# Kernel optimization log

Hardware: AMD Instinct MI355X
Metric: run time of the kernel (lower is better)

## Reference

```python
import jax, jax.numpy as jnp
from jax import lax
import numpy as np

T = 131072  # trajectory length


def _model_matrices():
    # F: constant-velocity model on augmented state [pose_t; pose_{t-1}]
    I6 = jnp.eye(6, dtype=jnp.float32)
    F = jnp.zeros((12, 12), dtype=jnp.float32)
    F = F.at[:6, :6].set(2.0 * I6)
    F = F.at[:6, 6:].set(-I6)
    F = F.at[6:, :6].set(I6)
    G = jnp.zeros((12, 6), dtype=jnp.float32)
    G = G.at[:6, :6].set(I6)
    return F, G


def setup_inputs() -> dict:
    key = jax.random.key(0)
    k1, = jax.random.split(key, 1)
    pose_measurements = jax.random.normal(k1, (T, 6), dtype=jnp.float32)
    # SPD noise covariances (scaled identities, as typical in the repo's config)
    process_noise_cov = 0.01 * jnp.eye(6, dtype=jnp.float32)
    measure_noise_cov = 0.05 * jnp.eye(6, dtype=jnp.float32)
    cov_init = jnp.eye(12, dtype=jnp.float32)  # _covariance_matrix_pred buffer
    return {
        "pose_measurements": pose_measurements,
        "process_noise_cov": process_noise_cov,
        "measure_noise_cov": measure_noise_cov,
        "cov_init": cov_init,
    }


def reference(pose_measurements, process_noise_cov, measure_noise_cov, cov_init):
    F, G = _model_matrices()
    Q_aug = G @ process_noise_cov @ G.T  # [[Q, 0], [0, 0]]  (12,12)
    I12 = jnp.eye(12, dtype=jnp.float32)
    z6 = jnp.zeros((12, 6), dtype=jnp.float32)

    def step(carry, meas):
        est, P = carry  # est: (12,), P: (12,12)
        # _predict
        v = est[:6] - est[6:]
        pred = jnp.concatenate([est[:6] + v, est[:6]])  # (12,)
        Pp = F @ P @ F.T + Q_aug
        # _update
        S = Pp[:6, :6] + measure_noise_cov            # (6,6)
        K = Pp[:, :6] @ jnp.linalg.inv(S)             # (12,6)
        est_new = pred + K @ (meas - pred[:6])        # (12,)
        KH = jnp.concatenate([K, z6], axis=1)         # (12,12)
        P_new = (I12 - KH) @ Pp
        return (est_new, P_new), (pred, est_new)

    # rows 0,1 initialized from measurements
    row0 = jnp.concatenate([pose_measurements[0], jnp.zeros(6, dtype=jnp.float32)])
    row1 = jnp.concatenate([pose_measurements[1], pose_measurements[0]])

    (_, _), (preds, ests) = lax.scan(step, (row1, cov_init), pose_measurements[2:])

    head = jnp.stack([row0, row1])                   # (2,12)
    pose_estimate = jnp.concatenate([head, ests], axis=0)    # (T,12)
    pose_prediction = jnp.concatenate([head, preds], axis=0)  # (T,12)
    velocity_estimate = pose_estimate[1:-1, :6] - pose_estimate[1:-1, 6:]

    return (pose_estimate[:, :6], pose_prediction[:, :6], velocity_estimate)
```

## Files before the change

kernel.cpp:

```cpp
#include <hip/hip_runtime.h>

#define T_LEN   131072
#define NSTEPS  (T_LEN - 2)
#define CHUNK   16
#define NCHUNK  8192
#define NCJ     (NCHUNK * 6)
#define CAP     512
#define CPB     128
#define NBLK    (NCHUNK / CPB)
#define K2T     (CPB * 6)

#define OFF_STEADY 16
#define OFF_K1     32
#define OFF_K2     (OFF_K1 + CAP * 4)
#define OFF_LP     (OFF_K2 + CAP * 4)
#define OFF_BT     (OFF_LP + NCHUNK * 16 * 4)
#define OFF_BI     (OFF_BT + NBLK * 16 * 4)

__global__ __launch_bounds__(64) void k_gains(
    const float* __restrict__ pnc, const float* __restrict__ mnc,
    const float* __restrict__ cov, float* __restrict__ ws_f,
    int* __restrict__ ws_i) {
    if (threadIdx.x != 0 || blockIdx.x != 0) return;
    float q = pnc[0];
    float r = mnc[0];
    float a = cov[0];
    float b = cov[6];
    float c = cov[6 * 12 + 6];
    float* k1a = ws_f + OFF_K1 / 4;
    float* k2a = ws_f + OFF_K2 / 4;
    float pk1 = -1e30f, pk2 = -1e30f;
    float k1 = 0.f, k2 = 0.f;
    int stable = 0;
    int s;
    for (s = 0; s < CAP; ++s) {
        float bp = 2.0f * a - b;
        float t2 = 2.0f * b - c;
        float ap = 2.0f * bp - t2 + q;
        float cp = a;
        float S  = ap + r;
        float invS = 1.0f / S;
        k1 = ap * invS;
        k2 = bp * invS;
        k1a[s] = k1;
        k2a[s] = k2;
        float om = 1.0f - k1;
        a = om * ap;
        b = om * bp;
        c = cp - k2 * bp;
        if (fabsf(k1 - pk1) <= 5e-7f * fabsf(k1) &&
            fabsf(k2 - pk2) <= 5e-7f * (fabsf(k2) + 1e-20f)) {
            if (++stable >= 8) { ++s; break; }
        } else {
            stable = 0;
        }
        pk1 = k1; pk2 = k2;
    }
    ws_i[0] = s;
    ws_f[OFF_STEADY / 4]     = k1;
    ws_f[OFF_STEADY / 4 + 1] = k2;
}

__device__ __forceinline__ void load_gains(int s, int sc, const float* k1a,
                                           const float* k2a, float k1s, float k2s,
                                           float& g1, float& g2) {
    int si = (s < sc) ? s : 0;
    float a = k1a[si], b = k2a[si];
    g1 = (s < sc) ? a : k1s;
    g2 = (s < sc) ? b : k2s;
}

__global__ __launch_bounds__(K2T) void k_chunk_scan(
    const float* __restrict__ meas, const float* __restrict__ ws_f,
    const int* __restrict__ ws_i, float* __restrict__ lp,
    float* __restrict__ btot) {
    __shared__ float lm[CPB][5];
    __shared__ float lu[CPB][13];
    int tid = threadIdx.x;
    int cl = tid / 6;
    int j  = tid - 6 * cl;
    int b  = blockIdx.x;
    int c  = b * CPB + cl;
    int sc = ws_i[0];
    float k1s = ws_f[OFF_STEADY / 4], k2s = ws_f[OFF_STEADY / 4 + 1];
    const float* k1a = ws_f + OFF_K1 / 4;
    const float* k2a = ws_f + OFF_K2 / 4;
    int s0 = c * CHUNK;
    float m00 = 1.f, m01 = 0.f, m10 = 0.f, m11 = 1.f;
    float u0 = 0.f, u1 = 0.f;
#pragma unroll
    for (int i = 0; i < CHUNK; ++i) {
        int s = s0 + i;
        if (s < NSTEPS) {
            float g1, g2;
            load_gains(s, sc, k1a, k2a, k1s, k2s, g1, g2);
            float om  = 1.0f - g1;
            float a00 = 2.0f * om, a01 = -om;
            float a10 = 1.0f - 2.0f * g2, a11 = g2;
            float n00 = a00 * m00 + a01 * m10;
            float n01 = a00 * m01 + a01 * m11;
            float n10 = a10 * m00 + a11 * m10;
            float n11 = a10 * m01 + a11 * m11;
            m00 = n00; m01 = n01; m10 = n10; m11 = n11;
            float mj = meas[(s + 2) * 6 + j];
            float v0 = a00 * u0 + a01 * u1 + g1 * mj;
            float v1 = a10 * u0 + a11 * u1 + g2 * mj;
            u0 = v0; u1 = v1;
        }
    }
    if (j == 0) { lm[cl][0] = m00; lm[cl][1] = m01; lm[cl][2] = m10; lm[cl][3] = m11; }
    lu[cl][j] = u0; lu[cl][6 + j] = u1;
    __syncthreads();
    for (int off = 1; off < CPB; off <<= 1) {
        bool act = (cl >= off);
        float M0, M1, M2, M3, P0, P1, P2, P3, pu0, pu1;
        if (act) {
            M0 = lm[cl][0]; M1 = lm[cl][1]; M2 = lm[cl][2]; M3 = lm[cl][3];
            P0 = lm[cl - off][0]; P1 = lm[cl - off][1];
            P2 = lm[cl - off][2]; P3 = lm[cl - off][3];
            pu0 = lu[cl - off][j]; pu1 = lu[cl - off][6 + j];
        }
        __syncthreads();
        if (act) {
            float nu0 = M0 * pu0 + M1 * pu1 + u0;
            float nu1 = M2 * pu0 + M3 * pu1 + u1;
            u0 = nu0; u1 = nu1;
            lu[cl][j] = u0; lu[cl][6 + j] = u1;
            if (j == 0) {
                lm[cl][0] = M0 * P0 + M1 * P2; lm[cl][1] = M0 * P1 + M1 * P3;
                lm[cl][2] = M2 * P0 + M3 * P2; lm[cl][3] = M2 * P1 + M3 * P3;
            }
        }
        __syncthreads();
    }
    for (int w = tid; w < CPB * 16; w += K2T) {
        int cc = w >> 4, k = w & 15;
        float v = (k < 4) ? lm[cc][k] : lu[cc][k - 4];
        lp[(b * CPB + cc) * 16 + k] = v;
    }
    if (tid < 16) {
        float v = (tid < 4) ? lm[CPB - 1][tid] : lu[CPB - 1][tid - 4];
        btot[b * 16 + tid] = v;
    }
}

__device__ __forceinline__ void compose(const float* L, const float* E, float* D) {
    float n00 = L[0] * E[0] + L[1] * E[2];
    float n01 = L[0] * E[1] + L[1] * E[3];
    float n10 = L[2] * E[0] + L[3] * E[2];
    float n11 = L[2] * E[1] + L[3] * E[3];
#pragma unroll
    for (int j = 0; j < 6; ++j) {
        float e0 = E[4 + j], e1 = E[10 + j];
        D[4 + j]  = L[0] * e0 + L[1] * e1 + L[4 + j];
        D[10 + j] = L[2] * e0 + L[3] * e1 + L[10 + j];
    }
    D[0] = n00; D[1] = n01; D[2] = n10; D[3] = n11;
}

__global__ __launch_bounds__(64) void k_bscan(const float* __restrict__ btot,
                                             float* __restrict__ binc) {
    __shared__ float ld[NBLK * 16];
    int t = threadIdx.x;
    float S[16];
#pragma unroll
    for (int k = 0; k < 16; ++k) { S[k] = btot[t * 16 + k]; ld[t * 16 + k] = S[k]; }
    __syncthreads();
    for (int off = 1; off < NBLK; off <<= 1) {
        bool act = (t >= off);
        float P[16];
        if (act) {
#pragma unroll
            for (int k = 0; k < 16; ++k) P[k] = ld[(t - off) * 16 + k];
        }
        __syncthreads();
        if (act) {
            float D[16];
            compose(S, P, D);
#pragma unroll
            for (int k = 0; k < 16; ++k) { S[k] = D[k]; ld[t * 16 + k] = S[k]; }
        }
        __syncthreads();
    }
#pragma unroll
    for (int k = 0; k < 16; ++k) binc[t * 16 + k] = S[k];
}

__global__ __launch_bounds__(256) void k_emit(
    const float* __restrict__ meas, const float* __restrict__ ws_f,
    const int* __restrict__ ws_i, const float* __restrict__ lp,
    const float* __restrict__ binc, float* __restrict__ out) {
    int g = blockIdx.x * 256 + threadIdx.x;
    if (g >= NCJ) return;
    int c = g / 6;
    int j = g - 6 * c;
    int b = c >> 7, cl = c & (CPB - 1);
    float* est  = out;
    float* pred = out + T_LEN * 6;
    float* vel  = out + T_LEN * 12;
    if (c == 0) {
        float m0 = meas[j], m1 = meas[6 + j];
        est[j] = m0; est[6 + j] = m1;
        pred[j] = m0; pred[6 + j] = m1;
        vel[j] = m1 - m0;
    }
    float zx = meas[6 + j], zy = meas[j];
    if (b > 0) {
        const float* B = binc + (b - 1) * 16;
        float nx = B[0] * zx + B[1] * zy + B[4 + j];
        float ny = B[2] * zx + B[3] * zy + B[10 + j];
        zx = nx; zy = ny;
    }
    if (cl > 0) {
        const float* L = lp + (c - 1) * 16;
        float nx = L[0] * zx + L[1] * zy + L[4 + j];
        float ny = L[2] * zx + L[3] * zy + L[10 + j];
        zx = nx; zy = ny;
    }
    float x = zx, y = zy;
    int sc = ws_i[0];
    float k1s = ws_f[OFF_STEADY / 4], k2s = ws_f[OFF_STEADY / 4 + 1];
    const float* k1a = ws_f + OFF_K1 / 4;
    const float* k2a = ws_f + OFF_K2 / 4;
    int s0 = c * CHUNK;
#pragma unroll
    for (int i = 0; i < CHUNK; ++i) {
        int s = s0 + i;
        if (s < NSTEPS) {
            float g1, g2;
            load_gains(s, sc, k1a, k2a, k1s, k2s, g1, g2);
            float mj  = meas[(s + 2) * 6 + j];
            float vx  = x - y;
            float p   = x + vx;
            float inn = mj - p;
            float xn  = p + g1 * inn;
            float yn  = x + g2 * inn;
            est[(s + 2) * 6 + j]  = xn;
            pred[(s + 2) * 6 + j] = p;
            if (s < NSTEPS - 1) vel[(s + 1) * 6 + j] = xn - yn;
            x = xn; y = yn;
        }
    }
}

extern "C" void kernel_launch(void* const* d_in, const int* in_sizes, int n_in,
                              void* d_out, int out_size, void* d_ws, size_t ws_size,
                              hipStream_t stream) {
    const float* meas = (const float*)d_in[0];
    const float* pnc  = (const float*)d_in[1];
    const float* mnc  = (const float*)d_in[2];
    const float* cov  = (const float*)d_in[3];
    float* ws_f = (float*)d_ws;
    int*   ws_i = (int*)d_ws;
    float* lp   = ws_f + OFF_LP / 4;
    float* btot = ws_f + OFF_BT / 4;
    float* binc = ws_f + OFF_BI / 4;
    float* out  = (float*)d_out;

    k_gains<<<1, 64, 0, stream>>>(pnc, mnc, cov, ws_f, ws_i);
    k_chunk_scan<<<NBLK, K2T, 0, stream>>>(meas, ws_f, ws_i, lp, btot);
    k_bscan<<<1, NBLK, 0, stream>>>(btot, binc);
    k_emit<<<NCJ / 256, 256, 0, stream>>>(meas, ws_f, ws_i, lp, binc, out);
}
```

Baseline: 84.22 us.

## Fuse Riccati gain computation into chunk scan and halve chunks per block

Removes the separate single-thread gain kernel. Each chunk-scan block now runs the Riccati recursion redundantly in thread 0 and keeps the gain table in shared memory. Only block 0 reads the transient gains and writes the tables to the workspace for the emit kernel; later blocks use the steady-state gains directly. Chunks per block drop from 128 to 64, which doubles the scan block count and the block-level prefix scan width. This saves a kernel launch and global gain loads, at the cost of a serial recursion inside every block.

```diff
diff --git a/kernel.cpp b/kernel.cpp
--- a/kernel.cpp
+++ b/kernel.cpp
@@ -6,7 +6,7 @@
 #define NCHUNK  8192
 #define NCJ     (NCHUNK * 6)
 #define CAP     512
-#define CPB     128
+#define CPB     64
 #define NBLK    (NCHUNK / CPB)
 #define K2T     (CPB * 6)
 
@@ -17,22 +17,13 @@
 #define OFF_BT     (OFF_LP + NCHUNK * 16 * 4)
 #define OFF_BI     (OFF_BT + NBLK * 16 * 4)
 
-__global__ __launch_bounds__(64) void k_gains(
-    const float* __restrict__ pnc, const float* __restrict__ mnc,
-    const float* __restrict__ cov, float* __restrict__ ws_f,
-    int* __restrict__ ws_i) {
-    if (threadIdx.x != 0 || blockIdx.x != 0) return;
-    float q = pnc[0];
-    float r = mnc[0];
-    float a = cov[0];
-    float b = cov[6];
-    float c = cov[6 * 12 + 6];
-    float* k1a = ws_f + OFF_K1 / 4;
-    float* k2a = ws_f + OFF_K2 / 4;
-    float pk1 = -1e30f, pk2 = -1e30f;
-    float k1 = 0.f, k2 = 0.f;
-    int stable = 0;
-    int s;
+__device__ __forceinline__ int riccati(const float* pnc, const float* mnc,
+                                       const float* cov, float* g1t, float* g2t,
+                                       float& k1o, float& k2o) {
+    float q = pnc[0], r = mnc[0];
+    float a = cov[0], b = cov[6], c = cov[6 * 12 + 6];
+    float pk1 = -1e30f, pk2 = -1e30f, k1 = 0.f, k2 = 0.f;
+    int stable = 0, s;
     for (s = 0; s < CAP; ++s) {
         float bp = 2.0f * a - b;
         float t2 = 2.0f * b - c;
@@ -42,8 +33,8 @@
         float invS = 1.0f / S;
         k1 = ap * invS;
         k2 = bp * invS;
-        k1a[s] = k1;
-        k2a[s] = k2;
+        g1t[s] = k1;
+        g2t[s] = k2;
         float om = 1.0f - k1;
         a = om * ap;
         b = om * bp;
@@ -56,35 +47,44 @@
         }
         pk1 = k1; pk2 = k2;
     }
-    ws_i[0] = s;
-    ws_f[OFF_STEADY / 4]     = k1;
-    ws_f[OFF_STEADY / 4 + 1] = k2;
-}
-
-__device__ __forceinline__ void load_gains(int s, int sc, const float* k1a,
-                                           const float* k2a, float k1s, float k2s,
-                                           float& g1, float& g2) {
-    int si = (s < sc) ? s : 0;
-    float a = k1a[si], b = k2a[si];
-    g1 = (s < sc) ? a : k1s;
-    g2 = (s < sc) ? b : k2s;
+    k1o = k1; k2o = k2;
+    return s;
 }
 
 __global__ __launch_bounds__(K2T) void k_chunk_scan(
-    const float* __restrict__ meas, const float* __restrict__ ws_f,
-    const int* __restrict__ ws_i, float* __restrict__ lp,
-    float* __restrict__ btot) {
+    const float* __restrict__ meas, const float* __restrict__ pnc,
+    const float* __restrict__ mnc, const float* __restrict__ cov,
+    float* __restrict__ ws_f, int* __restrict__ ws_i,
+    float* __restrict__ lp, float* __restrict__ btot) {
+    __shared__ float g1t[CAP], g2t[CAP];
     __shared__ float lm[CPB][5];
     __shared__ float lu[CPB][13];
+    __shared__ int   s_sc;
+    __shared__ float s_k1, s_k2;
     int tid = threadIdx.x;
     int cl = tid / 6;
     int j  = tid - 6 * cl;
     int b  = blockIdx.x;
-    int c  = b * CPB + cl;
-    int sc = ws_i[0];
-    float k1s = ws_f[OFF_STEADY / 4], k2s = ws_f[OFF_STEADY / 4 + 1];
-    const float* k1a = ws_f + OFF_K1 / 4;
-    const float* k2a = ws_f + OFF_K2 / 4;
+    if (tid == 0) {
+        float k1, k2;
+        int sc = riccati(pnc, mnc, cov, g1t, g2t, k1, k2);
+        s_sc = sc; s_k1 = k1; s_k2 = k2;
+    }
+    __syncthreads();
+    int sc = s_sc;
+    float k1s = s_k1, k2s = s_k2;
+    if (b == 0) {
+        for (int t = tid; t < sc; t += K2T) {
+            ws_f[OFF_K1 / 4 + t] = g1t[t];
+            ws_f[OFF_K2 / 4 + t] = g2t[t];
+        }
+        if (tid == 0) {
+            ws_i[0] = sc;
+            ws_f[OFF_STEADY / 4]     = k1s;
+            ws_f[OFF_STEADY / 4 + 1] = k2s;
+        }
+    }
+    int c = b * CPB + cl;
     int s0 = c * CHUNK;
     float m00 = 1.f, m01 = 0.f, m10 = 0.f, m11 = 1.f;
     float u0 = 0.f, u1 = 0.f;
@@ -93,7 +93,14 @@
         int s = s0 + i;
         if (s < NSTEPS) {
             float g1, g2;
-            load_gains(s, sc, k1a, k2a, k1s, k2s, g1, g2);
+            if (b == 0) {
+                int si = (s < sc) ? s : 0;
+                float ta = g1t[si], tb = g2t[si];
+                g1 = (s < sc) ? ta : k1s;
+                g2 = (s < sc) ? tb : k2s;
+            } else {
+                g1 = k1s; g2 = k2s;
+            }
             float om  = 1.0f - g1;
             float a00 = 2.0f * om, a01 = -om;
             float a10 = 1.0f - 2.0f * g2, a11 = g2;
@@ -158,8 +165,8 @@
     D[0] = n00; D[1] = n01; D[2] = n10; D[3] = n11;
 }
 
-__global__ __launch_bounds__(64) void k_bscan(const float* __restrict__ btot,
-                                             float* __restrict__ binc) {
+__global__ __launch_bounds__(NBLK) void k_bscan(const float* __restrict__ btot,
+                                                float* __restrict__ binc) {
     __shared__ float ld[NBLK * 16];
     int t = threadIdx.x;
     float S[16];
@@ -184,6 +191,15 @@
     }
 #pragma unroll
     for (int k = 0; k < 16; ++k) binc[t * 16 + k] = S[k];
+}
+
+__device__ __forceinline__ void load_gains(int s, int sc, const float* k1a,
+                                           const float* k2a, float k1s, float k2s,
+                                           float& g1, float& g2) {
+    int si = (s < sc) ? s : 0;
+    float a = k1a[si], b = k2a[si];
+    g1 = (s < sc) ? a : k1s;
+    g2 = (s < sc) ? b : k2s;
 }
 
 __global__ __launch_bounds__(256) void k_emit(
@@ -194,7 +210,7 @@
     if (g >= NCJ) return;
     int c = g / 6;
     int j = g - 6 * c;
-    int b = c >> 7, cl = c & (CPB - 1);
+    int b = c / CPB, cl = c & (CPB - 1);
     float* est  = out;
     float* pred = out + T_LEN * 6;
     float* vel  = out + T_LEN * 12;
@@ -257,8 +273,7 @@
     float* binc = ws_f + OFF_BI / 4;
     float* out  = (float*)d_out;
 
-    k_gains<<<1, 64, 0, stream>>>(pnc, mnc, cov, ws_f, ws_i);
-    k_chunk_scan<<<NBLK, K2T, 0, stream>>>(meas, ws_f, ws_i, lp, btot);
+    k_chunk_scan<<<NBLK, K2T, 0, stream>>>(meas, pnc, mnc, cov, ws_f, ws_i, lp, btot);
     k_bscan<<<1, NBLK, 0, stream>>>(btot, binc);
     k_emit<<<NCJ / 256, 256, 0, stream>>>(meas, ws_f, ws_i, lp, binc, out);
 }
```

Result: faster. 82.32 us (-2.3%).
